# Kernel optimization log

Hardware: AMD Instinct MI355X
Metric: run time of the kernel (lower is better)

The kernel has to match this reference:

```python
import jax, jax.numpy as jnp
import numpy as np

L = 8       # num_layers
D = 512     # embed_dim
H = 8       # num_heads
HD = D // H # head_dim = 64
V = 256     # vocab_size
T = 2048    # seq len (= context_length)
B = 4       # batch
FF = 4 * D  # mlp hidden
EPS = 1e-5


def setup_inputs() -> dict:
    key = jax.random.key(0)
    ks = jax.random.split(key, 18)
    g = lambda k, shape: (jax.random.normal(k, shape, jnp.float32) * 0.02)
    return {
        "x": jax.random.randint(ks[0], (B, T), 0, V),
        "tok_emb": g(ks[1], (V, D)),
        "pos_emb": g(ks[2], (T, D)),
        "attn_w": g(ks[3], (L, D, 3 * D)),
        "attn_b": g(ks[4], (L, 3 * D)),
        "proj_w": g(ks[5], (L, D, D)),
        "proj_b": g(ks[6], (L, D)),
        "ln1_g": jnp.ones((L, D), jnp.float32),
        "ln1_b": jnp.zeros((L, D), jnp.float32),
        "ln2_g": jnp.ones((L, D), jnp.float32),
        "ln2_b": jnp.zeros((L, D), jnp.float32),
        "ff1_w": g(ks[7], (L, D, FF)),
        "ff1_b": g(ks[8], (L, FF)),
        "ff2_w": g(ks[9], (L, FF, D)),
        "ff2_b": g(ks[10], (L, D)),
        "lnf_g": jnp.ones((D,), jnp.float32),
        "lnf_b": jnp.zeros((D,), jnp.float32),
    }


def _ln(x, g, b):
    m = jnp.mean(x, axis=-1, keepdims=True)
    v = jnp.mean(jnp.square(x - m), axis=-1, keepdims=True)
    return (x - m) * jax.lax.rsqrt(v + EPS) * g + b


def reference(x, tok_emb, pos_emb, attn_w, attn_b, proj_w, proj_b,
              ln1_g, ln1_b, ln2_g, ln2_b, ff1_w, ff1_b, ff2_w, ff2_b,
              lnf_g, lnf_b):
    Bx, Tx = x.shape
    h = tok_emb[x] + pos_emb[:Tx]                     # [B,T,D]
    causal = jnp.tril(jnp.ones((Tx, Tx), bool))       # [T,T]
    scale = 1.0 / np.sqrt(HD)
    for i in range(L):
        hn = _ln(h, ln1_g[i], ln1_b[i])
        qkv = hn @ attn_w[i] + attn_b[i]              # [B,T,3D]
        qkv = qkv.reshape(Bx, Tx, 3, H, HD)
        q = qkv[:, :, 0].transpose(0, 2, 1, 3)        # [B,H,T,HD]
        k = qkv[:, :, 1].transpose(0, 2, 1, 3)
        v = qkv[:, :, 2].transpose(0, 2, 1, 3)
        scores = jnp.einsum('bhqd,bhkd->bhqk', q, k) * scale
        scores = jnp.where(causal, scores, jnp.float32(-1e9))
        attn = jax.nn.softmax(scores, axis=-1)        # dropout identity at eval
        o = jnp.einsum('bhqk,bhkd->bhqd', attn, v)
        o = o.transpose(0, 2, 1, 3).reshape(Bx, Tx, D)
        h = h + o @ proj_w[i] + proj_b[i]
        hn2 = _ln(h, ln2_g[i], ln2_b[i])
        ff = jax.nn.gelu(hn2 @ ff1_w[i] + ff1_b[i], approximate=False)
        h = h + ff @ ff2_w[i] + ff2_b[i]
    logits = _ln(h, lnf_g, lnf_b) @ tok_emb.T         # tied lm_head
    return logits
```

## Files before the change

### kernel.cpp

```cpp
#include <hip/hip_runtime.h>

#define TT 2048
#define BB 4
#define DD 512
#define HH 8
#define LL 8
#define FFD 2048
#define VV 256
#define ROWS (BB*TT)

typedef short bf16x4 __attribute__((ext_vector_type(4)));
typedef short bf16x8 __attribute__((ext_vector_type(8)));
typedef float f32x4 __attribute__((ext_vector_type(4)));

#define GL2LDS(gp, lp) __builtin_amdgcn_global_load_lds( \
    (const __attribute__((address_space(1))) unsigned*)(gp), \
    (__attribute__((address_space(3))) unsigned*)(lp), 16, 0, 0)

__device__ __forceinline__ float bf2f(short s){
  union { unsigned u; float f; } x; x.u = ((unsigned)(unsigned short)s) << 16; return x.f;
}
__device__ __forceinline__ short f2bf(float f){
  union { float f; unsigned u; } x; x.f = f;
  unsigned r = (x.u + 0x7fffu + ((x.u >> 16) & 1u)) >> 16;
  return (short)(unsigned short)r;
}
__device__ __forceinline__ float ex2(float x){
  float r; asm("v_exp_f32 %0, %1" : "=v"(r) : "v"(x)); return r;
}
__device__ __forceinline__ unsigned cvtpk(float lo, float hi){
  unsigned r; asm("v_cvt_pk_bf16_f32 %0, %1, %2" : "=v"(r) : "v"(lo), "v"(hi)); return r;
}
__device__ __forceinline__ float xmax32(float x){ return fmaxf(x, __shfl_xor(x, 32)); }
__device__ __forceinline__ float xadd32(float x){ return x + __shfl_xor(x, 32); }

__global__ __launch_bounds__(128) void embed_kernel(const int* __restrict__ x,
    const float* __restrict__ tok, const float* __restrict__ pos, float* __restrict__ h){
  int row = blockIdx.x;
  int t = row & (TT-1);
  int id = x[row];
  const float4 a = *(const float4*)&tok[(size_t)id*DD + threadIdx.x*4];
  const float4 p = *(const float4*)&pos[(size_t)t*DD + threadIdx.x*4];
  float4 r; r.x=a.x+p.x; r.y=a.y+p.y; r.z=a.z+p.z; r.w=a.w+p.w;
  *(float4*)&h[(size_t)row*DD + threadIdx.x*4] = r;
}

__global__ __launch_bounds__(256) void ln_kernel(const float* __restrict__ xx,
    const float* __restrict__ gw, const float* __restrict__ bw, short* __restrict__ out){
  const int lane = threadIdx.x & 63, w = threadIdx.x >> 6;
  const int row = blockIdx.x*4 + w;
  const float* xp = xx + (size_t)row*DD + lane*8;
  float4 a = *(const float4*)xp, c = *(const float4*)(xp+4);
  float xv[8] = {a.x,a.y,a.z,a.w,c.x,c.y,c.z,c.w};
  float s1 = 0.f, s2 = 0.f;
  #pragma unroll
  for (int e=0;e<8;e++){ s1 += xv[e]; s2 += xv[e]*xv[e]; }
  #pragma unroll
  for (int off=1; off<64; off<<=1){
    s1 += __shfl_xor(s1, off);
    s2 += __shfl_xor(s2, off);
  }
  const float m = s1 * (1.0f/DD);
  const float rstd = rsqrtf(s2*(1.0f/DD) - m*m + 1e-5f);
  const float4 g0 = *(const float4*)(gw + lane*8), g1 = *(const float4*)(gw + lane*8 + 4);
  const float4 b0 = *(const float4*)(bw + lane*8), b1 = *(const float4*)(bw + lane*8 + 4);
  float gg[8] = {g0.x,g0.y,g0.z,g0.w,g1.x,g1.y,g1.z,g1.w};
  float bb[8] = {b0.x,b0.y,b0.z,b0.w,b1.x,b1.y,b1.z,b1.w};
  short r[8];
  #pragma unroll
  for (int e=0;e<8;e++) r[e] = f2bf((xv[e]-m)*rstd*gg[e] + bb[e]);
  *(bf16x8*)&out[(size_t)row*DD + lane*8] = *(const bf16x8*)r;
}

__global__ __launch_bounds__(256) void transpose_cast_kernel(const float* __restrict__ src,
    short* __restrict__ dst, int R, int C){
  __shared__ float tile[32][33];
  size_t off = (size_t)blockIdx.z * R * C;
  src += off; dst += off;
  int c0 = blockIdx.x*32, r0 = blockIdx.y*32;
  int tx = threadIdx.x & 31, ty = threadIdx.x >> 5;
  #pragma unroll
  for (int i=0;i<4;i++) tile[ty + i*8][tx] = src[(size_t)(r0+ty+i*8)*C + c0 + tx];
  __syncthreads();
  #pragma unroll
  for (int i=0;i<4;i++) dst[(size_t)(c0+ty+i*8)*R + r0 + tx] = f2bf(tile[tx][ty+i*8]);
}

__global__ void cast_kernel(const float* __restrict__ in, short* __restrict__ out, int n){
  for (int i = blockIdx.x*blockDim.x + threadIdx.x; i < n; i += gridDim.x*blockDim.x)
    out[i] = f2bf(in[i]);
}

__device__ __forceinline__ void xcd_rowband(int gx, int gy, int& rowt, int& colt){
  int lin = blockIdx.y*gx + blockIdx.x;
  int x = lin & 7, j = lin >> 3;
  int jd = j / gy;
  rowt = x*(gx >> 3) + jd;
  colt = j - jd*gy;
}

template<int EPI>
__global__ __launch_bounds__(256) void gemm_dma(const short* __restrict__ A,
    const short* __restrict__ BT, const float* __restrict__ bias, void* __restrict__ C,
    int M, int N, int K)
{
  __shared__ short As[2][128*64];
  __shared__ short Bs[2][128*64];
  int rowt, colt;
  xcd_rowband(gridDim.x, gridDim.y, rowt, colt);
  const int row0 = rowt*128, col0 = colt*128;
  const int t = threadIdx.x, lane = t & 63, w = t >> 6;
  const int wm = w >> 1, wn = w & 1;
  const int rr = lane & 15, g = lane >> 4;
  f32x4 acc[4][4];
  #pragma unroll
  for (int m=0;m<4;m++)
    #pragma unroll
    for (int n=0;n<4;n++) acc[m][n] = (f32x4){0.f,0.f,0.f,0.f};

  const short* aP = A  + (size_t)(row0 + w*32 + (lane>>3))*K + (lane&7)*8;
  const short* bP = BT + (size_t)(col0 + w*32 + (lane>>3))*K + (lane&7)*8;

  const int nk = K >> 6;
  #pragma unroll
  for (int i=0;i<4;i++){
    GL2LDS(aP + (size_t)i*8*K, &As[0][w*2048 + i*512]);
    GL2LDS(bP + (size_t)i*8*K, &Bs[0][w*2048 + i*512]);
  }
  for (int kt=0; kt<nk; kt++){
    asm volatile("s_waitcnt vmcnt(0) lgkmcnt(0)\n\ts_barrier" ::: "memory");
    if (kt+1 < nk){
      const int ko = (kt+1) << 6, nb = (kt+1) & 1;
      #pragma unroll
      for (int i=0;i<4;i++){
        GL2LDS(aP + (size_t)i*8*K + ko, &As[nb][w*2048 + i*512]);
        GL2LDS(bP + (size_t)i*8*K + ko, &Bs[nb][w*2048 + i*512]);
      }
    }
    const short* Ac = As[kt&1];
    const short* Bc = Bs[kt&1];
    #pragma unroll
    for (int ks=0; ks<2; ks++){
      bf16x8 af[4], bfr[4];
      #pragma unroll
      for (int m=0;m<4;m++) af[m]  = *(const bf16x8*)&Ac[(wm*64 + m*16 + rr)*64 + ks*32 + g*8];
      #pragma unroll
      for (int n=0;n<4;n++) bfr[n] = *(const bf16x8*)&Bc[(wn*64 + n*16 + rr)*64 + ks*32 + g*8];
      #pragma unroll
      for (int m=0;m<4;m++)
        #pragma unroll
        for (int n=0;n<4;n++)
          acc[m][n] = __builtin_amdgcn_mfma_f32_16x16x32_bf16(af[m], bfr[n], acc[m][n], 0,0,0);
    }
  }
  #pragma unroll
  for (int m=0;m<4;m++){
    #pragma unroll
    for (int n=0;n<4;n++){
      int cg = col0 + wn*64 + n*16 + rr;
      float bv = bias[cg];
      #pragma unroll
      for (int i=0;i<4;i++){
        int rg = row0 + wm*64 + m*16 + g*4 + i;
        float v = acc[m][n][i] + bv;
        size_t idx = (size_t)rg*N + cg;
        if constexpr (EPI==1) ((short*)C)[idx] = f2bf(v);
        else if constexpr (EPI==2) { v = 0.5f*v*(1.0f + erff(v*0.70710678118f)); ((short*)C)[idx] = f2bf(v); }
        else { ((float*)C)[idx] += v; }
      }
    }
  }
}

__global__ __launch_bounds__(256) void gemm_dma_n64(const short* __restrict__ A,
    const short* __restrict__ BT, const float* __restrict__ bias, float* __restrict__ C,
    int M, int N, int K)
{
  __shared__ short As[128*64];
  __shared__ short Bs[64*64];
  int rowt, colt;
  xcd_rowband(gridDim.x, gridDim.y, rowt, colt);
  const int row0 = rowt*128, col0 = colt*64;
  const int t = threadIdx.x, lane = t & 63, w = t >> 6;
  const int wm = w >> 1, wn = w & 1;
  const int rr = lane & 15, g = lane >> 4;
  f32x4 acc[4][2];
  #pragma unroll
  for (int m=0;m<4;m++)
    #pragma unroll
    for (int n=0;n<2;n++) acc[m][n] = (f32x4){0.f,0.f,0.f,0.f};

  const short* aP = A  + (size_t)(row0 + w*32 + (lane>>3))*K + (lane&7)*8;
  const short* bP = BT + (size_t)(col0 + w*16 + (lane>>3))*K + (lane&7)*8;
  short* aL = As + w*2048;
  short* bL = Bs + w*1024;

  for (int kt=0; kt<K; kt+=64){
    __syncthreads();
    #pragma unroll
    for (int i=0;i<4;i++) GL2LDS(aP + (size_t)i*8*K + kt, aL + i*512);
    #pragma unroll
    for (int i=0;i<2;i++) GL2LDS(bP + (size_t)i*8*K + kt, bL + i*512);
    __syncthreads();
    #pragma unroll
    for (int ks=0; ks<2; ks++){
      bf16x8 af[4], bfr[2];
      #pragma unroll
      for (int m=0;m<4;m++) af[m]  = *(const bf16x8*)&As[(wm*64 + m*16 + rr)*64 + ks*32 + g*8];
      #pragma unroll
      for (int n=0;n<2;n++) bfr[n] = *(const bf16x8*)&Bs[(wn*32 + n*16 + rr)*64 + ks*32 + g*8];
      #pragma unroll
      for (int m=0;m<4;m++)
        #pragma unroll
        for (int n=0;n<2;n++)
          acc[m][n] = __builtin_amdgcn_mfma_f32_16x16x32_bf16(af[m], bfr[n], acc[m][n], 0,0,0);
    }
  }
  #pragma unroll
  for (int m=0;m<4;m++){
    #pragma unroll
    for (int n=0;n<2;n++){
      int cg = col0 + wn*32 + n*16 + rr;
      float bv = bias[cg];
      #pragma unroll
      for (int i=0;i<4;i++){
        int rg = row0 + wm*64 + m*16 + g*4 + i;
        C[(size_t)rg*N + cg] += acc[m][n][i] + bv;
      }
    }
  }
}

template<int BM, int BN>
__global__ __launch_bounds__(256) void gemm_small(const short* __restrict__ A,
    const short* __restrict__ BT, float* __restrict__ C, int M, int N, int K)
{
  constexpr int FM = BM/32, FN = BN/32;
  __shared__ short As[BM][72];
  __shared__ short Bs[BN][72];
  const int row0 = blockIdx.x*BM, col0 = blockIdx.y*BN;
  const int t = threadIdx.x, lane = t & 63, w = t >> 6;
  const int wm = w >> 1, wn = w & 1;
  const int rr = lane & 15, kg = (lane >> 4)*8;
  f32x4 acc[FM][FN];
  #pragma unroll
  for (int m=0;m<FM;m++)
    #pragma unroll
    for (int n=0;n<FN;n++) acc[m][n] = (f32x4){0.f,0.f,0.f,0.f};

  for (int kt=0; kt<K; kt+=64){
    #pragma unroll
    for (int i=0;i<BM/32;i++){
      int cid = t + i*256; int r = cid >> 3; int c = (cid & 7)*8;
      *(bf16x8*)&As[r][c] = *(const bf16x8*)&A[(size_t)(row0+r)*K + kt + c];
    }
    #pragma unroll
    for (int i=0;i<BN/32;i++){
      int cid = t + i*256; int r = cid >> 3; int c = (cid & 7)*8;
      *(bf16x8*)&Bs[r][c] = *(const bf16x8*)&BT[(size_t)(col0+r)*K + kt + c];
    }
    __syncthreads();
    #pragma unroll
    for (int ks=0; ks<2; ks++){
      bf16x8 af[FM], bfr[FN];
      #pragma unroll
      for (int m=0;m<FM;m++) af[m] = *(const bf16x8*)&As[wm*FM*16 + m*16 + rr][ks*32 + kg];
      #pragma unroll
      for (int n=0;n<FN;n++) bfr[n] = *(const bf16x8*)&Bs[wn*FN*16 + n*16 + rr][ks*32 + kg];
      #pragma unroll
      for (int m=0;m<FM;m++)
        #pragma unroll
        for (int n=0;n<FN;n++)
          acc[m][n] = __builtin_amdgcn_mfma_f32_16x16x32_bf16(af[m], bfr[n], acc[m][n], 0,0,0);
    }
    __syncthreads();
  }
  #pragma unroll
  for (int m=0;m<FM;m++)
    #pragma unroll
    for (int n=0;n<FN;n++){
      int cg = col0 + wn*FN*16 + n*16 + rr;
      #pragma unroll
      for (int i=0;i<4;i++){
        int rg = row0 + wm*FM*16 + m*16 + (lane>>4)*4 + i;
        C[(size_t)rg*N + cg] = acc[m][n][i];
      }
    }
}

__device__ __forceinline__ void attn_tile(const short* __restrict__ Kc,
    const short* __restrict__ Vc, const bf16x8* qr, f32x4* oacc,
    float& mrun, float& lpart, int qi, int g, int qloc, bool diag)
{
  f32x4 sacc[4];
  #pragma unroll
  for (int f=0; f<4; f++) sacc[f] = (f32x4){0.f,0.f,0.f,0.f};
  __builtin_amdgcn_s_setprio(1);
  #pragma unroll
  for (int ks=0; ks<2; ks++){
    #pragma unroll
    for (int f=0; f<4; f++){
      bf16x8 kf = *(const bf16x8*)&Kc[(f*16 + qi)*64 + (((ks*4 + g) ^ (qi&7))*8)];
      sacc[f] = __builtin_amdgcn_mfma_f32_16x16x32_bf16(kf, qr[ks], sacc[f], 0,0,0);
    }
  }
  __builtin_amdgcn_s_setprio(0);

  float p[4][4];
  if (diag){
    #pragma unroll
    for (int f=0; f<4; f++)
      #pragma unroll
      for (int i=0; i<4; i++){
        int koffs = f*16 + g*4 + i;
        p[f][i] = (koffs <= qloc) ? sacc[f][i] : -1e30f;
      }
  } else {
    #pragma unroll
    for (int f=0; f<4; f++)
      #pragma unroll
      for (int i=0; i<4; i++) p[f][i] = sacc[f][i];
  }
  float t0 = fmaxf(fmaxf(p[0][0],p[0][1]), fmaxf(p[0][2],p[0][3]));
  float t1 = fmaxf(fmaxf(p[1][0],p[1][1]), fmaxf(p[1][2],p[1][3]));
  float t2 = fmaxf(fmaxf(p[2][0],p[2][1]), fmaxf(p[2][2],p[2][3]));
  float t3 = fmaxf(fmaxf(p[3][0],p[3][1]), fmaxf(p[3][2],p[3][3]));
  float tm = fmaxf(fmaxf(t0,t1), fmaxf(t2,t3));
  tm = fmaxf(tm, __shfl_xor(tm, 16));
  tm = xmax32(tm);
  if (!__all(tm <= mrun + 8.f)){
    float mnew = fmaxf(mrun, tm);
    float corr = ex2(mrun - mnew);
    lpart *= corr;
    #pragma unroll
    for (int mf=0; mf<4; mf++)
      #pragma unroll
      for (int i=0; i<4; i++) oacc[mf][i] *= corr;
    mrun = mnew;
  }
  float ts = 0.f;
  #pragma unroll
  for (int f=0; f<4; f++)
    #pragma unroll
    for (int i=0; i<4; i++){
      float e = ex2(p[f][i] - mrun);
      p[f][i] = e;
      ts += e;
    }
  lpart += ts;

  __builtin_amdgcn_s_setprio(1);
  #pragma unroll
  for (int w2=0; w2<2; w2++){
    union { unsigned u[4]; bf16x8 v; } bfr;
    bfr.u[0] = cvtpk(p[2*w2  ][0], p[2*w2  ][1]);
    bfr.u[1] = cvtpk(p[2*w2  ][2], p[2*w2  ][3]);
    bfr.u[2] = cvtpk(p[2*w2+1][0], p[2*w2+1][1]);
    bfr.u[3] = cvtpk(p[2*w2+1][2], p[2*w2+1][3]);
    #pragma unroll
    for (int mf=0; mf<4; mf++){
      const short* vp = &Vc[(mf*16 + qi)*72 + w2*32 + g*4];
      union { bf16x4 h[2]; bf16x8 v; } af;
      af.h[0] = *(const bf16x4*)vp;
      af.h[1] = *(const bf16x4*)(vp + 16);
      oacc[mf] = __builtin_amdgcn_mfma_f32_16x16x32_bf16(af.v, bfr.v, oacc[mf], 0,0,0);
    }
  }
  __builtin_amdgcn_s_setprio(0);
}

__global__ __launch_bounds__(256) void attn_kernel(const short* __restrict__ qkv, short* __restrict__ o){
  __shared__ __align__(16) char smem[34816];
  short* KsB = (short*)smem;
  short* VtB = (short*)(smem + 16384);
  float* Osh = (float*)smem;

  const int lin = blockIdx.x;
  const int xcd = lin & 7, idx = lin >> 3;
  const int bh = xcd*4 + (idx & 3);
  const int qp = idx >> 2;
  const int b = bh >> 3, hh = bh & 7;
  const int ql = qp, qh = 31 - qp;
  const int nt = qh + 1;

  const int t = threadIdx.x, lane = t & 63, wid = t >> 6;
  const int g = lane >> 4, qi = lane & 15;
  const int qloc = wid*16 + qi;
  const size_t base = (size_t)b*TT*3*DD + hh*64;

  bf16x8 qL[2], qH[2];
  {
    const float qs = 0.125f * 1.44269504f;
    const short* qpL = qkv + base + (size_t)(ql*64 + qloc)*3*DD + g*8;
    const short* qpH = qkv + base + (size_t)(qh*64 + qloc)*3*DD + g*8;
    qL[0] = *(const bf16x8*)&qpL[0]; qL[1] = *(const bf16x8*)&qpL[32];
    qH[0] = *(const bf16x8*)&qpH[0]; qH[1] = *(const bf16x8*)&qpH[32];
    #pragma unroll
    for (int j=0;j<8;j++){
      qL[0][j] = f2bf(qs * bf2f(qL[0][j]));
      qL[1][j] = f2bf(qs * bf2f(qL[1][j]));
      qH[0][j] = f2bf(qs * bf2f(qH[0][j]));
      qH[1][j] = f2bf(qs * bf2f(qH[1][j]));
    }
  }
  f32x4 oL[4], oH[4];
  #pragma unroll
  for (int mf=0; mf<4; mf++){ oL[mf] = (f32x4){0.f,0.f,0.f,0.f}; oH[mf] = (f32x4){0.f,0.f,0.f,0.f}; }
  float mL = -1e30f, lL = 0.f, mH = -1e30f, lH = 0.f;

  const short* ksrc = qkv + base + DD + (size_t)(wid*16 + (lane>>3))*3*DD
                      + (((lane&7) ^ (lane>>3))*8);
  const int vk = (t & 31)*2, vd = (t >> 5)*8;
  const short* vsrc = qkv + base + 2*DD + (size_t)vk*3*DD + vd;

  GL2LDS(ksrc, KsB + wid*1024);
  GL2LDS(ksrc + (size_t)8*3*DD, KsB + wid*1024 + 512);
  bf16x8 v0a = *(const bf16x8*)vsrc;
  bf16x8 v0b = *(const bf16x8*)(vsrc + 3*DD);
  bf16x8 vLoA = *(const bf16x8*)(vsrc + (size_t)64*3*DD);
  bf16x8 vLoB = *(const bf16x8*)(vsrc + (size_t)64*3*DD + 3*DD);
  asm volatile("s_waitcnt vmcnt(0)" ::: "memory");
  #pragma unroll
  for (int e=0;e<8;e++)
    *(unsigned*)&VtB[(vd+e)*72 + vk] =
        (unsigned)(unsigned short)v0a[e] | ((unsigned)(unsigned short)v0b[e] << 16);

  for (int kb = 0; kb < nt; kb++){
    asm volatile("s_waitcnt vmcnt(0) lgkmcnt(0)\n\ts_barrier" ::: "memory");
    bf16x8 vHiA = vLoA, vHiB = vLoB;
    if (kb+1 < nt){
      const size_t koff = (size_t)(kb+1)*64*3*DD;
      short* kd = KsB + ((kb+1)&1)*4096 + wid*1024;
      GL2LDS(ksrc + koff, kd);
      GL2LDS(ksrc + koff + (size_t)8*3*DD, kd + 512);
      short* Vn = VtB + ((kb+1)&1)*4608;
      #pragma unroll
      for (int e=0;e<8;e++)
        *(unsigned*)&Vn[(vd+e)*72 + vk] =
            (unsigned)(unsigned short)vLoA[e] | ((unsigned)(unsigned short)vLoB[e] << 16);
    }
    if (kb+2 < nt){
      const size_t koff2 = (size_t)(kb+2)*64*3*DD;
      vHiA = *(const bf16x8*)(vsrc + koff2);
      vHiB = *(const bf16x8*)(vsrc + koff2 + 3*DD);
    }
    const short* Kc = KsB + (kb&1)*4096;
    const short* Vc = VtB + (kb&1)*4608;

    attn_tile(Kc, Vc, qH, oH, mH, lH, qi, g, qloc, kb == nt-1);
    if (kb <= ql)
      attn_tile(Kc, Vc, qL, oL, mL, lL, qi, g, qloc, kb == ql);

    vLoA = vHiA; vLoB = vHiB;
  }

  lL += __shfl_xor(lL, 16); lL = xadd32(lL);
  lH += __shfl_xor(lH, 16); lH = xadd32(lH);

  const int orow = t >> 2, cc = (t & 3) * 16;
  #pragma unroll
  for (int s=0; s<2; s++){
    const f32x4* oacc = s ? oH : oL;
    const float inv = 1.f / (s ? lH : lL);
    const int q0 = (s ? qh : ql) * 64;
    __syncthreads();
    #pragma unroll
    for (int mf=0; mf<4; mf++)
      #pragma unroll
      for (int i=0; i<4; i++)
        Osh[qloc*65 + mf*16 + g*4 + i] = oacc[mf][i] * inv;
    __syncthreads();
    short tmp[16];
    #pragma unroll
    for (int e=0; e<16; e++) tmp[e] = f2bf(Osh[orow*65 + cc + e]);
    short* op = o + ((size_t)b*TT + q0 + orow)*DD + hh*64 + cc;
    *(bf16x8*)&op[0] = *(const bf16x8*)&tmp[0];
    *(bf16x8*)&op[8] = *(const bf16x8*)&tmp[8];
  }
}

extern "C" void kernel_launch(void* const* d_in, const int* in_sizes, int n_in,
                              void* d_out, int out_size, void* d_ws, size_t ws_size,
                              hipStream_t stream) {
  const int*   x      = (const int*)d_in[0];
  const float* tok    = (const float*)d_in[1];
  const float* pos    = (const float*)d_in[2];
  const float* attn_w = (const float*)d_in[3];
  const float* attn_b = (const float*)d_in[4];
  const float* proj_w = (const float*)d_in[5];
  const float* proj_b = (const float*)d_in[6];
  const float* ln1_g  = (const float*)d_in[7];
  const float* ln1_b  = (const float*)d_in[8];
  const float* ln2_g  = (const float*)d_in[9];
  const float* ln2_b  = (const float*)d_in[10];
  const float* ff1_w  = (const float*)d_in[11];
  const float* ff1_b  = (const float*)d_in[12];
  const float* ff2_w  = (const float*)d_in[13];
  const float* ff2_b  = (const float*)d_in[14];
  const float* lnf_g  = (const float*)d_in[15];
  const float* lnf_b  = (const float*)d_in[16];

  char* p = (char*)d_ws;
  float* h   = (float*)p; p += (size_t)ROWS*DD*4;
  short* hn  = (short*)p; p += (size_t)ROWS*DD*2;
  short* qkv = (short*)p; p += (size_t)ROWS*3*DD*2;
  short* ob  = (short*)p; p += (size_t)ROWS*DD*2;
  short* ffb = (short*)p; p += (size_t)ROWS*FFD*2;
  short* awT = (short*)p; p += (size_t)LL*3*DD*DD*2;
  short* pwT = (short*)p; p += (size_t)LL*DD*DD*2;
  short* f1T = (short*)p; p += (size_t)LL*FFD*DD*2;
  short* f2T = (short*)p; p += (size_t)LL*DD*FFD*2;
  short* lmT = (short*)p; p += (size_t)VV*DD*2;

  transpose_cast_kernel<<<dim3(48,16,8),256,0,stream>>>(attn_w, awT, DD, 3*DD);
  transpose_cast_kernel<<<dim3(16,16,8),256,0,stream>>>(proj_w, pwT, DD, DD);
  transpose_cast_kernel<<<dim3(64,16,8),256,0,stream>>>(ff1_w, f1T, DD, FFD);
  transpose_cast_kernel<<<dim3(16,64,8),256,0,stream>>>(ff2_w, f2T, FFD, DD);
  cast_kernel<<<128,256,0,stream>>>(tok, lmT, VV*DD);
  embed_kernel<<<ROWS,128,0,stream>>>(x, tok, pos, h);

  for (int l=0;l<LL;l++){
    ln_kernel<<<ROWS/4,256,0,stream>>>(h, ln1_g + l*DD, ln1_b + l*DD, hn);
    gemm_dma<1><<<dim3(ROWS/128, (3*DD)/128),256,0,stream>>>(
        hn, awT + (size_t)l*3*DD*DD, attn_b + (size_t)l*3*DD, qkv, ROWS, 3*DD, DD);
    attn_kernel<<<512,256,0,stream>>>(qkv, ob);
    gemm_dma_n64<<<dim3(ROWS/128, DD/64),256,0,stream>>>(
        ob, pwT + (size_t)l*DD*DD, proj_b + (size_t)l*DD, h, ROWS, DD, DD);
    ln_kernel<<<ROWS/4,256,0,stream>>>(h, ln2_g + l*DD, ln2_b + l*DD, hn);
    gemm_dma<2><<<dim3(ROWS/128, FFD/128),256,0,stream>>>(
        hn, f1T + (size_t)l*FFD*DD, ff1_b + (size_t)l*FFD, ffb, ROWS, FFD, DD);
    gemm_dma_n64<<<dim3(ROWS/128, DD/64),256,0,stream>>>(
        ffb, f2T + (size_t)l*DD*FFD, ff2_b + (size_t)l*DD, h, ROWS, DD, FFD);
  }
  ln_kernel<<<ROWS/4,256,0,stream>>>(h, lnf_g, lnf_b, hn);
  gemm_small<64,64><<<dim3(ROWS/64, VV/64),256,0,stream>>>(
      hn, lmT, (float*)d_out, ROWS, VV, DD);
}
```

Before: 1.572 ms.

## Deepen GEMM prefetch to two stages, double-buffer n64 GEMM, approximate GELU erf

The main GEMM now issues loads two k-tiles ahead and waits with partial vmcnt, so the next tile's DMA overlaps compute instead of draining every iteration. The n64 GEMM gains a double-buffered LDS pipeline with the same scheme in place of its single-buffer load-sync-compute loop. The GELU epilogue replaces erff with an Abramowitz-Stegun polynomial using hardware exp2, which is cheaper but has an approximation error of about 1e-7. The extra LDS buffer lowers occupancy headroom, and the vmcnt counts must match the number of outstanding loads exactly.

```diff
diff --git a/kernel.cpp b/kernel.cpp
--- a/kernel.cpp
+++ b/kernel.cpp
@@ -33,6 +33,17 @@
 }
 __device__ __forceinline__ float xmax32(float x){ return fmaxf(x, __shfl_xor(x, 32)); }
 __device__ __forceinline__ float xadd32(float x){ return x + __shfl_xor(x, 32); }
+
+__device__ __forceinline__ float gelu_f(float v){
+  float x = v * 0.70710678118f;
+  float a = fabsf(x);
+  float t = 1.0f / (1.0f + 0.3275911f * a);
+  float poly = t*(0.254829592f + t*(-0.284496736f + t*(1.421413741f +
+               t*(-1.453152027f + t*1.061405429f))));
+  float er = 1.0f - poly * ex2(-1.44269504f * a * a);
+  er = (x < 0.f) ? -er : er;
+  return 0.5f * v * (1.0f + er);
+}
 
 __global__ __launch_bounds__(128) void embed_kernel(const int* __restrict__ x,
     const float* __restrict__ tok, const float* __restrict__ pos, float* __restrict__ h){
@@ -127,30 +138,39 @@
     GL2LDS(aP + (size_t)i*8*K, &As[0][w*2048 + i*512]);
     GL2LDS(bP + (size_t)i*8*K, &Bs[0][w*2048 + i*512]);
   }
+  if (nk > 1){
+    #pragma unroll
+    for (int i=0;i<4;i++){
+      GL2LDS(aP + (size_t)i*8*K + 64, &As[1][w*2048 + i*512]);
+      GL2LDS(bP + (size_t)i*8*K + 64, &Bs[1][w*2048 + i*512]);
+    }
+  }
   for (int kt=0; kt<nk; kt++){
-    asm volatile("s_waitcnt vmcnt(0) lgkmcnt(0)\n\ts_barrier" ::: "memory");
-    if (kt+1 < nk){
-      const int ko = (kt+1) << 6, nb = (kt+1) & 1;
+    if (kt < nk-1) asm volatile("s_waitcnt vmcnt(8)\n\ts_barrier" ::: "memory");
+    else           asm volatile("s_waitcnt vmcnt(0)\n\ts_barrier" ::: "memory");
+    const short* Ac = As[kt&1];
+    const short* Bc = Bs[kt&1];
+    #pragma unroll
+    for (int ks=0; ks<2; ks++){
+      bf16x8 af[4], bfr[4];
+      #pragma unroll
+      for (int m=0;m<4;m++) af[m]  = *(const bf16x8*)&Ac[(wm*64 + m*16 + rr)*64 + ks*32 + g*8];
+      #pragma unroll
+      for (int n=0;n<4;n++) bfr[n] = *(const bf16x8*)&Bc[(wn*64 + n*16 + rr)*64 + ks*32 + g*8];
+      #pragma unroll
+      for (int m=0;m<4;m++)
+        #pragma unroll
+        for (int n=0;n<4;n++)
+          acc[m][n] = __builtin_amdgcn_mfma_f32_16x16x32_bf16(af[m], bfr[n], acc[m][n], 0,0,0);
+    }
+    asm volatile("s_waitcnt lgkmcnt(0)\n\ts_barrier" ::: "memory");
+    if (kt+2 < nk){
+      const int ko = (kt+2) << 6, nb = kt & 1;
       #pragma unroll
       for (int i=0;i<4;i++){
         GL2LDS(aP + (size_t)i*8*K + ko, &As[nb][w*2048 + i*512]);
         GL2LDS(bP + (size_t)i*8*K + ko, &Bs[nb][w*2048 + i*512]);
       }
-    }
-    const short* Ac = As[kt&1];
-    const short* Bc = Bs[kt&1];
-    #pragma unroll
-    for (int ks=0; ks<2; ks++){
-      bf16x8 af[4], bfr[4];
-      #pragma unroll
-      for (int m=0;m<4;m++) af[m]  = *(const bf16x8*)&Ac[(wm*64 + m*16 + rr)*64 + ks*32 + g*8];
-      #pragma unroll
-      for (int n=0;n<4;n++) bfr[n] = *(const bf16x8*)&Bc[(wn*64 + n*16 + rr)*64 + ks*32 + g*8];
-      #pragma unroll
-      for (int m=0;m<4;m++)
-        #pragma unroll
-        for (int n=0;n<4;n++)
-          acc[m][n] = __builtin_amdgcn_mfma_f32_16x16x32_bf16(af[m], bfr[n], acc[m][n], 0,0,0);
     }
   }
   #pragma unroll
@@ -165,8 +185,8 @@
         float v = acc[m][n][i] + bv;
         size_t idx = (size_t)rg*N + cg;
         if constexpr (EPI==1) ((short*)C)[idx] = f2bf(v);
-        else if constexpr (EPI==2) { v = 0.5f*v*(1.0f + erff(v*0.70710678118f)); ((short*)C)[idx] = f2bf(v); }
-        else { ((float*)C)[idx] += v; }
+        else if constexpr (EPI==2) ((short*)C)[idx] = f2bf(gelu_f(v));
+        else ((float*)C)[idx] += v;
       }
     }
   }
@@ -176,8 +196,8 @@
     const short* __restrict__ BT, const float* __restrict__ bias, float* __restrict__ C,
     int M, int N, int K)
 {
-  __shared__ short As[128*64];
-  __shared__ short Bs[64*64];
+  __shared__ short As[2][128*64];
+  __shared__ short Bs[2][64*64];
   int rowt, colt;
   xcd_rowband(gridDim.x, gridDim.y, rowt, colt);
   const int row0 = rowt*128, col0 = colt*64;
@@ -192,28 +212,43 @@
 
   const short* aP = A  + (size_t)(row0 + w*32 + (lane>>3))*K + (lane&7)*8;
   const short* bP = BT + (size_t)(col0 + w*16 + (lane>>3))*K + (lane&7)*8;
-  short* aL = As + w*2048;
-  short* bL = Bs + w*1024;
-
-  for (int kt=0; kt<K; kt+=64){
-    __syncthreads();
-    #pragma unroll
-    for (int i=0;i<4;i++) GL2LDS(aP + (size_t)i*8*K + kt, aL + i*512);
-    #pragma unroll
-    for (int i=0;i<2;i++) GL2LDS(bP + (size_t)i*8*K + kt, bL + i*512);
-    __syncthreads();
+
+  const int nk = K >> 6;
+  #pragma unroll
+  for (int i=0;i<4;i++) GL2LDS(aP + (size_t)i*8*K, &As[0][w*2048 + i*512]);
+  #pragma unroll
+  for (int i=0;i<2;i++) GL2LDS(bP + (size_t)i*8*K, &Bs[0][w*1024 + i*512]);
+  if (nk > 1){
+    #pragma unroll
+    for (int i=0;i<4;i++) GL2LDS(aP + (size_t)i*8*K + 64, &As[1][w*2048 + i*512]);
+    #pragma unroll
+    for (int i=0;i<2;i++) GL2LDS(bP + (size_t)i*8*K + 64, &Bs[1][w*1024 + i*512]);
+  }
+  for (int kt=0; kt<nk; kt++){
+    if (kt < nk-1) asm volatile("s_waitcnt vmcnt(6)\n\ts_barrier" ::: "memory");
+    else           asm volatile("s_waitcnt vmcnt(0)\n\ts_barrier" ::: "memory");
+    const short* Ac = As[kt&1];
+    const short* Bc = Bs[kt&1];
     #pragma unroll
     for (int ks=0; ks<2; ks++){
       bf16x8 af[4], bfr[2];
       #pragma unroll
-      for (int m=0;m<4;m++) af[m]  = *(const bf16x8*)&As[(wm*64 + m*16 + rr)*64 + ks*32 + g*8];
-      #pragma unroll
-      for (int n=0;n<2;n++) bfr[n] = *(const bf16x8*)&Bs[(wn*32 + n*16 + rr)*64 + ks*32 + g*8];
+      for (int m=0;m<4;m++) af[m]  = *(const bf16x8*)&Ac[(wm*64 + m*16 + rr)*64 + ks*32 + g*8];
+      #pragma unroll
+      for (int n=0;n<2;n++) bfr[n] = *(const bf16x8*)&Bc[(wn*32 + n*16 + rr)*64 + ks*32 + g*8];
       #pragma unroll
       for (int m=0;m<4;m++)
         #pragma unroll
         for (int n=0;n<2;n++)
           acc[m][n] = __builtin_amdgcn_mfma_f32_16x16x32_bf16(af[m], bfr[n], acc[m][n], 0,0,0);
+    }
+    asm volatile("s_waitcnt lgkmcnt(0)\n\ts_barrier" ::: "memory");
+    if (kt+2 < nk){
+      const int ko = (kt+2) << 6, nb = kt & 1;
+      #pragma unroll
+      for (int i=0;i<4;i++) GL2LDS(aP + (size_t)i*8*K + ko, &As[nb][w*2048 + i*512]);
+      #pragma unroll
+      for (int i=0;i<2;i++) GL2LDS(bP + (size_t)i*8*K + ko, &Bs[nb][w*1024 + i*512]);
     }
   }
   #pragma unroll
```

New measurement: 1.580 ms. About the same (+0.5%).
